# Kernel tuning notes

Measured on AMD Instinct MI355X. Metric: run time of the kernel, lower is better.

## Reference

```python
import jax, jax.numpy as jnp
import numpy as np

C = 256
R = 2
HEADS = 8
HEAD_DIM = C // HEADS
SCALE = HEAD_DIM ** -0.5
EPS = 1e-5


def setup_inputs() -> dict:
    key = jax.random.key(0)
    ks = jax.random.split(key, 7)
    x = jax.random.normal(ks[0], (8, C, 64, 64), dtype=jnp.float32)
    # qkv 1x1 conv weight [3C, C], no bias
    w_qkv = jax.random.normal(ks[1], (3 * C, C), dtype=jnp.float32) * (C ** -0.5)
    # depthwise ConvTranspose2d(C, C, k=r, stride=r, groups=C): weight [C, r, r], bias [C]
    w_lp = jax.random.normal(ks[2], (C, R, R), dtype=jnp.float32) * 0.5
    b_lp = jax.random.normal(ks[3], (C,), dtype=jnp.float32) * 0.01
    # GroupNorm(1, C) affine params
    gamma = jnp.ones((C,), dtype=jnp.float32)
    beta = jnp.zeros((C,), dtype=jnp.float32)
    # proj 1x1 conv weight [C, C], no bias
    w_proj = jax.random.normal(ks[4], (C, C), dtype=jnp.float32) * (C ** -0.5)
    return {"x": x, "w_qkv": w_qkv, "w_lp": w_lp, "b_lp": b_lp,
            "gamma": gamma, "beta": beta, "w_proj": w_proj}


def reference(x, w_qkv, w_lp, b_lp, gamma, beta, w_proj):
    # sparse_sampler: AvgPool2d(kernel=1, stride=r) == strided subsampling
    xs = x[:, :, ::R, ::R]                      # [B, C, H, W]
    B, _, H, W = xs.shape
    N = H * W
    # qkv 1x1 conv -> [B, 3C, N] -> [B, heads, 3*head_dim, N]
    qkv = jnp.einsum('oc,bcn->bon', w_qkv, xs.reshape(B, C, N))
    qkv = qkv.reshape(B, HEADS, 3 * HEAD_DIM, N)
    q, k, v = jnp.split(qkv, 3, axis=2)         # each [B, h, d, N]
    # attn[b,h,i,j] = softmax_j( (q^T k)[i,j] * scale )
    attn = jax.nn.softmax(jnp.einsum('bhdi,bhdj->bhij', q, k) * SCALE, axis=-1)
    # out[b,h,d,i] = sum_j v[b,h,d,j] attn[b,h,i,j]
    out = jnp.einsum('bhdj,bhij->bhdi', v, attn).reshape(B, C, H, W)
    # depthwise ConvTranspose2d kernel=r stride=r (non-overlapping): broadcast each
    # pixel into an r x r block weighted by the per-channel kernel, plus bias.
    up = jnp.einsum('bchw,cpq->bchpwq', out, w_lp).reshape(B, C, H * R, W * R)
    up = up + b_lp[None, :, None, None]
    # GroupNorm with 1 group: normalize over (C, H, W) per sample
    mu = jnp.mean(up, axis=(1, 2, 3), keepdims=True)
    var = jnp.var(up, axis=(1, 2, 3), keepdims=True)
    normed = (up - mu) * jax.lax.rsqrt(var + EPS)
    normed = normed * gamma[None, :, None, None] + beta[None, :, None, None]
    # proj 1x1 conv
    Bo, _, Ho, Wo = normed.shape
    y = jnp.einsum('oc,bcn->bon', w_proj, normed.reshape(Bo, C, Ho * Wo))
    return y.reshape(Bo, C, Ho, Wo)
```

## Files before the change

kernel.cpp:

```cpp
#include <hip/hip_runtime.h>
#include <hip/hip_bf16.h>

#define ATT_SCALE_L2E 0.2550322540f

typedef __attribute__((ext_vector_type(8))) short bf16x8;
typedef __attribute__((ext_vector_type(4))) short bf16x4;
typedef __attribute__((ext_vector_type(4))) float f32x4;
typedef __attribute__((ext_vector_type(16))) float f32x16;
typedef __attribute__((ext_vector_type(4))) int i32x4;

#define MFMA16(a, b, c) __builtin_amdgcn_mfma_f32_16x16x32_bf16(a, b, c, 0, 0, 0)
#define MFMA32(a, b, c) __builtin_amdgcn_mfma_f32_32x32x16_bf16(a, b, c, 0, 0, 0)

__device__ inline short f2b(float f) {
    return __builtin_bit_cast(short, __float2bfloat16(f));
}

__device__ inline int cvt_pk(float a, float b) {
    int r;
    asm("v_cvt_pk_bf16_f32 %0, %1, %2" : "=v"(r) : "v"(a), "v"(b));
    return r;
}

__global__ __launch_bounds__(256) void wconv_k(const float* __restrict__ w,
                                               short* __restrict__ wb) {
    int i0 = (blockIdx.x * 256 + threadIdx.x) * 8;
    float4 lo = *(const float4*)(w + i0);
    float4 hi = *(const float4*)(w + i0 + 4);
    bf16x8 o;
    o[0] = f2b(lo.x); o[1] = f2b(lo.y); o[2] = f2b(lo.z); o[3] = f2b(lo.w);
    o[4] = f2b(hi.x); o[5] = f2b(hi.y); o[6] = f2b(hi.z); o[7] = f2b(hi.w);
    *(bf16x8*)(wb + i0) = o;
}

__global__ __launch_bounds__(256) void xt_k(const float* __restrict__ x,
                                            short* __restrict__ xt) {
    int b = blockIdx.y;
    int t = threadIdx.x;
    int n = blockIdx.x * 32 + (t >> 3);
    const float* xb = x + (size_t)b * 1048576 + (n >> 5) * 128 + (n & 31) * 2;
    short* dst = xt + ((size_t)b * 1024 + n) * 256;
#pragma unroll
    for (int it = 0; it < 4; ++it) {
        int c = (t & 7) * 8 + it * 64;
        bf16x8 o;
#pragma unroll
        for (int j = 0; j < 8; ++j) o[j] = f2b(xb[(size_t)(c + j) * 4096]);
        *(bf16x8*)(dst + c) = o;
    }
}

__global__ __launch_bounds__(256) void qkv_k(const short* __restrict__ wb,
                                             const short* __restrict__ xt,
                                             short* __restrict__ qt,
                                             short* __restrict__ ktr,
                                             short* __restrict__ vvr) {
    int b = blockIdx.x;
    int ntile = blockIdx.y * 128;
    int otile = blockIdx.z * 64;
    int t = threadIdx.x;
    int w = t >> 6, l = t & 63, g = l >> 4, li = l & 15;
    int oh = (w & 1) * 32, mh = (w >> 1) * 64;
    int o_base = otile + oh;
    int head = o_base / 96;
    int role = (o_base >> 5) % 3;
    size_t bh = (size_t)b * 8 + head;

    const short* arow = wb + (size_t)o_base * 256;
    const short* brow = xt + ((size_t)b * 1024 + ntile + mh) * 256;

    f32x4 zero = {0.f, 0.f, 0.f, 0.f};
    f32x4 acc[2][4];
#pragma unroll
    for (int og = 0; og < 2; ++og)
#pragma unroll
        for (int mg = 0; mg < 4; ++mg) acc[og][mg] = zero;

#pragma unroll
    for (int kc = 0; kc < 256; kc += 32) {
        bf16x8 af[2], bf_[4];
#pragma unroll
        for (int og = 0; og < 2; ++og)
            af[og] = *(const bf16x8*)(arow + (size_t)(og * 16 + li) * 256 + kc + 8 * g);
#pragma unroll
        for (int mg = 0; mg < 4; ++mg)
            bf_[mg] = *(const bf16x8*)(brow + (size_t)(mg * 16 + li) * 256 + kc + 8 * g);
#pragma unroll
        for (int og = 0; og < 2; ++og)
#pragma unroll
            for (int mg = 0; mg < 4; ++mg)
                acc[og][mg] = MFMA16(af[og], bf_[mg], acc[og][mg]);
    }

    __shared__ short Tl[4][32][64];
    short (*Tw)[64] = Tl[w];
    float sc = (role == 0) ? ATT_SCALE_L2E : 1.f;

#pragma unroll
    for (int og = 0; og < 2; ++og)
#pragma unroll
        for (int mg = 0; mg < 4; ++mg)
#pragma unroll
            for (int r = 0; r < 4; ++r) {
                int op = og * 16 + 4 * g + r;
                int qp = (op >> 3) & 3;
                Tw[op][(mg * 16 + li) ^ (qp << 4)] = f2b(acc[og][mg][r] * sc);
            }
    __syncthreads();

    if (role == 0) {
#pragma unroll
        for (int it = 0; it < 4; ++it) {
            int s = it * 64 + l;
            int dq = (l & 3) * 8;
            int n = s >> 2;
            int q2 = dq >> 3;
            bf16x8 vo;
#pragma unroll
            for (int j = 0; j < 8; ++j)
                vo[j] = Tw[dq + j][n ^ (q2 << 4)];
            *(bf16x8*)(qt + ((size_t)bh * 1024 + ntile + mh + n) * 32 + dq) = vo;
        }
    } else if (role == 1) {
        int base_jb = (ntile + mh) >> 5;
#pragma unroll
        for (int it = 0; it < 4; ++it) {
            int s = it * 64 + l;
            int il2 = s & 31;
            int combo = (s >> 5) & 3;
            int jbr = s >> 7;
            int dq = combo * 8;
            int n_rel = jbr * 32 + il2;
            bf16x8 vo;
#pragma unroll
            for (int j = 0; j < 8; ++j)
                vo[j] = Tw[dq + j][n_rel ^ (combo << 4)];
            *(bf16x8*)(ktr + (size_t)bh * 32768 +
                       (size_t)(base_jb + jbr) * 1024 + combo * 256 + il2 * 8) = vo;
        }
    } else {
        int base_jb = (ntile + mh) >> 5;
#pragma unroll
        for (int it = 0; it < 4; ++it) {
            int s = it * 64 + l;
            int il2 = s & 31;
            int combo = (s >> 5) & 3;
            int jbr = s >> 7;
            int pan = combo >> 1, hi2 = combo & 1;
            int q2 = (il2 >> 3) & 3;
            int bn = jbr * 32 + pan * 16 + 4 * hi2;
            bf16x8 vo;
#pragma unroll
            for (int j = 0; j < 4; ++j) vo[j] = Tw[il2][(bn + j) ^ (q2 << 4)];
#pragma unroll
            for (int j = 0; j < 4; ++j) vo[4 + j] = Tw[il2][(bn + 8 + j) ^ (q2 << 4)];
            *(bf16x8*)(vvr + (size_t)bh * 32768 +
                       (size_t)(base_jb + jbr) * 1024 + combo * 256 + il2 * 8) = vo;
        }
    }
}

__global__ __launch_bounds__(256) void attn_k(const short* __restrict__ qt,
                                              const short* __restrict__ ktr,
                                              const short* __restrict__ vvr,
                                              float* __restrict__ ao2) {
    int bh = blockIdx.x;
    int b = bh >> 3, h = bh & 7;
    int w = threadIdx.x >> 6, l = threadIdx.x & 63;
    int il = l & 31, hi = l >> 5;
    int ibase = blockIdx.y * 128 + w * 32;

    const short* qtb = qt + (size_t)bh * 32768;
    const short* kbase = ktr + (size_t)bh * 32768 + hi * 256 + il * 8;
    const short* vbase = vvr + (size_t)bh * 32768 + hi * 256 + il * 8;

    bf16x8 qf0 = *(const bf16x8*)(qtb + (size_t)(ibase + il) * 32 + 8 * hi);
    bf16x8 qf1 = *(const bf16x8*)(qtb + (size_t)(ibase + il) * 32 + 16 + 8 * hi);

    f32x16 zero16 = {0.f,0.f,0.f,0.f,0.f,0.f,0.f,0.f,0.f,0.f,0.f,0.f,0.f,0.f,0.f,0.f};
    f32x16 oacc = zero16;
    float lr0 = 0.f, lr1 = 0.f, lr2 = 0.f, lr3 = 0.f;

#pragma unroll 2
    for (int jb = 0; jb < 32; ++jb) {
        const short* kp = kbase + (size_t)jb * 1024;
        const short* vp = vbase + (size_t)jb * 1024;
        bf16x8 kf0 = *(const bf16x8*)(kp);
        bf16x8 kf1 = *(const bf16x8*)(kp + 512);
        f32x16 s = MFMA32(kf0, qf0, zero16);
        s = MFMA32(kf1, qf1, s);

        float p[16];
#pragma unroll
        for (int r = 0; r < 16; ++r) p[r] = exp2f(s[r]);
        lr0 += p[0] + p[4] + p[8]  + p[12];
        lr1 += p[1] + p[5] + p[9]  + p[13];
        lr2 += p[2] + p[6] + p[10] + p[14];
        lr3 += p[3] + p[7] + p[11] + p[15];

        i32x4 fa, fb;
        fa[0] = cvt_pk(p[0], p[1]);   fa[1] = cvt_pk(p[2], p[3]);
        fa[2] = cvt_pk(p[4], p[5]);   fa[3] = cvt_pk(p[6], p[7]);
        fb[0] = cvt_pk(p[8], p[9]);   fb[1] = cvt_pk(p[10], p[11]);
        fb[2] = cvt_pk(p[12], p[13]); fb[3] = cvt_pk(p[14], p[15]);
        bf16x8 pfa = __builtin_bit_cast(bf16x8, fa);
        bf16x8 pfb = __builtin_bit_cast(bf16x8, fb);

        bf16x8 vfa = *(const bf16x8*)(vp);
        bf16x8 vfb = *(const bf16x8*)(vp + 512);
        oacc = MFMA32(vfa, pfa, oacc);
        oacc = MFMA32(vfb, pfb, oacc);
    }

    float lrun = (lr0 + lr1) + (lr2 + lr3);
    float tot = lrun + __shfl_xor(lrun, 32);
    float inv = 1.f / tot;

    float* base = ao2 + ((size_t)(b * 256 + h * 32)) * 1024 + ibase + il;
#pragma unroll
    for (int r = 0; r < 16; ++r) {
        int d = (r & 3) + 8 * (r >> 2) + 4 * hi;
        base[(size_t)d * 1024] = oacc[r] * inv;
    }
}

__global__ __launch_bounds__(64) void psum_k(const float* __restrict__ ao2,
                                             float* __restrict__ p1,
                                             float* __restrict__ p2) {
    int row = blockIdx.x;
    const float* base = ao2 + (size_t)row * 1024;
    int l = threadIdx.x;
    float s = 0.f, q = 0.f;
#pragma unroll
    for (int t = 0; t < 4; ++t) {
        float4 v = *(const float4*)(base + l * 4 + t * 256);
        s += v.x + v.y + v.z + v.w;
        q += v.x * v.x + v.y * v.y + v.z * v.z + v.w * v.w;
    }
#pragma unroll
    for (int o = 1; o < 64; o <<= 1) {
        s += __shfl_xor(s, o);
        q += __shfl_xor(q, o);
    }
    if (l == 0) { p1[row] = s; p2[row] = q; }
}

__global__ __launch_bounds__(256) void stats_k(const float* __restrict__ p1,
                                               const float* __restrict__ p2,
                                               const float* __restrict__ wlp,
                                               const float* __restrict__ blp,
                                               float* __restrict__ stats) {
    int b = blockIdx.x, c = threadIdx.x;
    float s = p1[b * 256 + c];
    float q = p2[b * 256 + c];
    float w0 = wlp[c * 4], w1 = wlp[c * 4 + 1], w2 = wlp[c * 4 + 2], w3 = wlp[c * 4 + 3];
    float S1 = w0 + w1 + w2 + w3, S2 = w0 * w0 + w1 * w1 + w2 * w2 + w3 * w3;
    float bl = blp[c];
    float su = S1 * s + 4096.f * bl;
    float sq = S2 * q + 2.f * bl * S1 * s + 4096.f * bl * bl;
    __shared__ float rs_[256], rq_[256];
    rs_[c] = su; rq_[c] = sq;
    __syncthreads();
    for (int o = 128; o > 0; o >>= 1) {
        if (c < o) { rs_[c] += rs_[c + o]; rq_[c] += rq_[c + o]; }
        __syncthreads();
    }
    if (c == 0) {
        const float N = 1048576.f;
        float mu = rs_[0] / N;
        float var = rq_[0] / N - mu * mu;
        stats[b] = mu;
        stats[8 + b] = rsqrtf(var + 1e-5f);
    }
}

__global__ __launch_bounds__(256) void proj_k(const float* __restrict__ ao2,
                                              const float* __restrict__ wp,
                                              const float* __restrict__ wlp,
                                              const float* __restrict__ blp,
                                              const float* __restrict__ gamma,
                                              const float* __restrict__ beta,
                                              const float* __restrict__ stats,
                                              float* __restrict__ y) {
    int b = blockIdx.x;
    int mt = blockIdx.y;
    int otile = blockIdx.z * 64;
    float mu = stats[b], rs = stats[8 + b];

    __shared__ short As[64][40];
    __shared__ short Bs[128][40];

    int t = threadIdx.x;
    int w = t >> 6, l = t & 63, g = l >> 4, li = l & 15;
    int oh = (w >> 1) * 32, mh = (w & 1) * 64;

    f32x4 zero = {0.f, 0.f, 0.f, 0.f};
    f32x4 acc[2][4];
#pragma unroll
    for (int og = 0; og < 2; ++og)
#pragma unroll
        for (int mg = 0; mg < 4; ++mg) acc[og][mg] = zero;

    int so = t >> 2, sc = (t & 3) * 8;
    int bc = t & 31, bm = (t >> 5) * 16;
    int p = t >> 7;
    int wbase = bm & 63;

    for (int kc = 0; kc < 256; kc += 32) {
        const float* wrow = wp + (size_t)(otile + so) * 256 + kc + sc;
#pragma unroll
        for (int j = 0; j < 8; ++j) As[so][sc + j] = f2b(wrow[j]);
        int c = kc + bc;
        float Ac = gamma[c] * rs;
        float Dc = Ac * (blp[c] - mu) + beta[c];
        float w0 = Ac * wlp[c * 4 + p * 2 + 0];
        float w1 = Ac * wlp[c * 4 + p * 2 + 1];
        const float* arow = ao2 + ((size_t)(b * 256 + c)) * 1024 + mt * 32 + (wbase >> 1);
        float4 a0 = *(const float4*)arow;
        float4 a1 = *(const float4*)(arow + 4);
        float av[8] = {a0.x, a0.y, a0.z, a0.w, a1.x, a1.y, a1.z, a1.w};
#pragma unroll
        for (int k = 0; k < 8; ++k) {
            Bs[bm + 2 * k    ][bc] = f2b(w0 * av[k] + Dc);
            Bs[bm + 2 * k + 1][bc] = f2b(w1 * av[k] + Dc);
        }
        __syncthreads();
        bf16x8 af[2], bf_[4];
#pragma unroll
        for (int og = 0; og < 2; ++og) af[og] = *(const bf16x8*)&As[oh + og * 16 + li][8 * g];
#pragma unroll
        for (int mg = 0; mg < 4; ++mg) bf_[mg] = *(const bf16x8*)&Bs[mh + mg * 16 + li][8 * g];
#pragma unroll
        for (int og = 0; og < 2; ++og)
#pragma unroll
            for (int mg = 0; mg < 4; ++mg) acc[og][mg] = MFMA16(af[og], bf_[mg], acc[og][mg]);
        __syncthreads();
    }

#pragma unroll
    for (int og = 0; og < 2; ++og) {
        int o = otile + oh + og * 16 + 4 * g;
#pragma unroll
        for (int mg = 0; mg < 4; ++mg) {
            int m = mt * 128 + mh + mg * 16 + li;
            float* yp = y + ((size_t)b * 256 + o) * 4096 + m;
#pragma unroll
            for (int r = 0; r < 4; ++r) yp[(size_t)r * 4096] = acc[og][mg][r];
        }
    }
}

extern "C" void kernel_launch(void* const* d_in, const int* in_sizes, int n_in,
                              void* d_out, int out_size, void* d_ws, size_t ws_size,
                              hipStream_t stream) {
    const float* x      = (const float*)d_in[0];
    const float* w_qkv  = (const float*)d_in[1];
    const float* w_lp   = (const float*)d_in[2];
    const float* b_lp   = (const float*)d_in[3];
    const float* gamma  = (const float*)d_in[4];
    const float* beta   = (const float*)d_in[5];
    const float* w_proj = (const float*)d_in[6];
    float* y = (float*)d_out;

    short* qt   = (short*)d_out;
    short* ktr  = qt + 2097152;
    short* vvr  = ktr + 2097152;
    short* xt   = vvr + 2097152;
    short* wbuf = xt + 2097152;

    float* ao2   = (float*)d_ws;
    float* p1    = ao2 + 2097152;
    float* p2    = p1 + 2048;
    float* stats = p2 + 2048;

    wconv_k<<<96, 256, 0, stream>>>(w_qkv, wbuf);
    xt_k<<<dim3(32, 8), 256, 0, stream>>>(x, xt);
    qkv_k<<<dim3(8, 8, 12), 256, 0, stream>>>(wbuf, xt, qt, ktr, vvr);
    attn_k<<<dim3(64, 8), 256, 0, stream>>>(qt, ktr, vvr, ao2);
    psum_k<<<2048, 64, 0, stream>>>(ao2, p1, p2);
    stats_k<<<8, 256, 0, stream>>>(p1, p2, w_lp, b_lp, stats);
    proj_k<<<dim3(8, 32, 4), 256, 0, stream>>>(ao2, w_proj, w_lp, b_lp, gamma, beta, stats, y);
}
```

Measured before the change: 83.63 us.

## Split attention key range across two wave groups and merge via LDS

The attention kernel now runs 512 threads per block. Two groups of four waves each process half of the 32 key blocks for the same query rows, and the partial outputs and row sums are combined through shared memory before the store. This doubles the wave count per block and halves each wave's serial loop, so the exp/MFMA chain has more latency hiding. In exchange it adds a block barrier, LDS traffic, and a second group of waves that sits idle during the final write.

```diff
diff --git a/kernel.cpp b/kernel.cpp
--- a/kernel.cpp
+++ b/kernel.cpp
@@ -160,19 +160,21 @@
     }
 }
 
-__global__ __launch_bounds__(256) void attn_k(const short* __restrict__ qt,
+__global__ __launch_bounds__(512) void attn_k(const short* __restrict__ qt,
                                               const short* __restrict__ ktr,
                                               const short* __restrict__ vvr,
                                               float* __restrict__ ao2) {
     int bh = blockIdx.x;
     int b = bh >> 3, h = bh & 7;
-    int w = threadIdx.x >> 6, l = threadIdx.x & 63;
+    int t = threadIdx.x;
+    int w = t >> 6, l = t & 63;
     int il = l & 31, hi = l >> 5;
-    int ibase = blockIdx.y * 128 + w * 32;
+    int wq = w & 3, jh = w >> 2;
+    int ibase = blockIdx.y * 128 + wq * 32;
 
     const short* qtb = qt + (size_t)bh * 32768;
-    const short* kbase = ktr + (size_t)bh * 32768 + hi * 256 + il * 8;
-    const short* vbase = vvr + (size_t)bh * 32768 + hi * 256 + il * 8;
+    const short* kbase = ktr + (size_t)bh * 32768 + jh * 16384 + hi * 256 + il * 8;
+    const short* vbase = vvr + (size_t)bh * 32768 + jh * 16384 + hi * 256 + il * 8;
 
     bf16x8 qf0 = *(const bf16x8*)(qtb + (size_t)(ibase + il) * 32 + 8 * hi);
     bf16x8 qf1 = *(const bf16x8*)(qtb + (size_t)(ibase + il) * 32 + 16 + 8 * hi);
@@ -182,7 +184,7 @@
     float lr0 = 0.f, lr1 = 0.f, lr2 = 0.f, lr3 = 0.f;
 
 #pragma unroll 2
-    for (int jb = 0; jb < 32; ++jb) {
+    for (int jb = 0; jb < 16; ++jb) {
         const short* kp = kbase + (size_t)jb * 1024;
         const short* vp = vbase + (size_t)jb * 1024;
         bf16x8 kf0 = *(const bf16x8*)(kp);
@@ -213,14 +215,32 @@
     }
 
     float lrun = (lr0 + lr1) + (lr2 + lr3);
-    float tot = lrun + __shfl_xor(lrun, 32);
-    float inv = 1.f / tot;
-
-    float* base = ao2 + ((size_t)(b * 256 + h * 32)) * 1024 + ibase + il;
-#pragma unroll
-    for (int r = 0; r < 16; ++r) {
-        int d = (r & 3) + 8 * (r >> 2) + 4 * hi;
-        base[(size_t)d * 1024] = oacc[r] * inv;
+
+    __shared__ float OB[4][64][20];
+    __shared__ float LB[4][32];
+
+    if (jh == 1) {
+#pragma unroll
+        for (int r4 = 0; r4 < 4; ++r4) {
+            float4 v = {oacc[r4 * 4], oacc[r4 * 4 + 1], oacc[r4 * 4 + 2], oacc[r4 * 4 + 3]};
+            *(float4*)&OB[wq][l][r4 * 4] = v;
+        }
+        float tu = lrun + __shfl_xor(lrun, 32);
+        if (hi == 0) LB[wq][il] = tu;
+    }
+    __syncthreads();
+    if (jh == 0) {
+#pragma unroll
+        for (int r = 0; r < 16; ++r) oacc[r] += OB[wq][l][r];
+        float tl = lrun + __shfl_xor(lrun, 32);
+        float inv = 1.f / (tl + LB[wq][il]);
+
+        float* base = ao2 + ((size_t)(b * 256 + h * 32)) * 1024 + ibase + il;
+#pragma unroll
+        for (int r = 0; r < 16; ++r) {
+            int d = (r & 3) + 8 * (r >> 2) + 4 * hi;
+            base[(size_t)d * 1024] = oacc[r] * inv;
+        }
     }
 }
 
@@ -376,7 +396,7 @@
     wconv_k<<<96, 256, 0, stream>>>(w_qkv, wbuf);
     xt_k<<<dim3(32, 8), 256, 0, stream>>>(x, xt);
     qkv_k<<<dim3(8, 8, 12), 256, 0, stream>>>(wbuf, xt, qt, ktr, vvr);
-    attn_k<<<dim3(64, 8), 256, 0, stream>>>(qt, ktr, vvr, ao2);
+    attn_k<<<dim3(64, 8), 512, 0, stream>>>(qt, ktr, vvr, ao2);
     psum_k<<<2048, 64, 0, stream>>>(ao2, p1, p2);
     stats_k<<<8, 256, 0, stream>>>(p1, p2, w_lp, b_lp, stats);
     proj_k<<<dim3(8, 32, 4), 256, 0, stream>>>(ao2, w_proj, w_lp, b_lp, gamma, beta, stats, y);
```

After: 78.68 us, median of 3. 5.9% less time.
